# Performance work log

Measured on AMD Instinct MI355X. Metric: run time of the kernel, lower is better.

## Reference

```python
import jax, jax.numpy as jnp
import numpy as np

C = 128; N = 2; H = 64; W = 64; NH = 8
DI = 128; DS = 16; DTR = 8
PE_TEMP = 0.01

def lrelu(x):
    return jnp.where(x >= 0, x, 0.1 * x)

def conv2d(x, w, b, pad):
    y = jax.lax.conv_general_dilated(x, w, (1, 1), [(pad, pad), (pad, pad)],
                                     dimension_numbers=('NCHW', 'OIHW', 'NCHW'))
    return y + b[None, :, None, None]

def _gather2d(img, yy, xx):
    # img (n,c,h,w); yy,xx int32 (n,h,w) -> (n,c,h,w)
    n, c, h, w = img.shape
    idx = (yy * w + xx).reshape(n, 1, h * w)
    g = jnp.take_along_axis(img.reshape(n, c, h * w),
                            jnp.broadcast_to(idx, (n, c, h * w)), axis=2)
    return g.reshape(n, c, h, w)

def bilinear_warp(img, flow):
    # flow (n,2,h,w): [dx, dy]
    n, c, h, w = img.shape
    gy, gx = jnp.meshgrid(jnp.arange(h, dtype=jnp.float32),
                          jnp.arange(w, dtype=jnp.float32), indexing='ij')
    x = gx[None] + flow[:, 0]; y = gy[None] + flow[:, 1]
    x0 = jnp.floor(x); y0 = jnp.floor(y)
    dx = x - x0; dy = y - y0
    x0c = jnp.clip(x0, 0, w - 1).astype(jnp.int32)
    x1c = jnp.clip(x0 + 1, 0, w - 1).astype(jnp.int32)
    y0c = jnp.clip(y0, 0, h - 1).astype(jnp.int32)
    y1c = jnp.clip(y0 + 1, 0, h - 1).astype(jnp.int32)
    wa = ((1 - dx) * (1 - dy))[:, None]; wb = ((1 - dx) * dy)[:, None]
    wc = (dx * (1 - dy))[:, None]; wd = (dx * dy)[:, None]
    return (wa * _gather2d(img, y0c, x0c) + wb * _gather2d(img, y1c, x0c)
            + wc * _gather2d(img, y0c, x1c) + wd * _gather2d(img, y1c, x1c))

def posenc(rel, dim, temp=PE_TEMP):
    # rel (...,2) -> (...,dim) sinusoidal PE with temperature pe_temp
    d4 = dim // 4
    omega = temp ** (jnp.arange(d4, dtype=jnp.float32) / d4)
    xx = rel[..., 0:1] * omega
    yy = rel[..., 1:2] * omega
    return jnp.concatenate([jnp.sin(xx), jnp.cos(xx), jnp.sin(yy), jnp.cos(yy)], axis=-1)

def spynet_flow(f1, f2, s1w, s1b, s2w, s2b, levels=3):
    # SpyNet-style coarse-to-fine residual flow estimation (frozen weights)
    p1 = [f1]; p2 = [f2]
    for _ in range(levels - 1):
        a = p1[-1]; n, c, h, w = a.shape
        p1.append(a.reshape(n, c, h // 2, 2, w // 2, 2).mean(axis=(3, 5)))
        b_ = p2[-1]
        p2.append(b_.reshape(n, c, h // 2, 2, w // 2, 2).mean(axis=(3, 5)))
    flow = None
    for lvl in range(levels - 1, -1, -1):
        a = p1[lvl]; b_ = p2[lvl]
        n, c, h, w = a.shape
        if flow is None:
            flow = jnp.zeros((n, 2, h, w), jnp.float32)
        else:
            flow = 2.0 * jax.image.resize(flow, (n, 2, h, w), 'bilinear')
        warped = bilinear_warp(b_, flow)
        inp = jnp.concatenate([a, warped, flow], axis=1)
        hh = lrelu(conv2d(inp, s1w, s1b, 1))
        flow = flow + conv2d(hh, s2w, s2b, 1)
    return flow

def implicit_warp(feat_prop, feat_cur, flow, wqw, wqb, wkw, wkb, wvw, wvb, wow, wob):
    # Implicit attention-based warp: for each query pixel, attend over the 4
    # integer neighbors of its flow-displaced position in feat_prop, with
    # sinusoidal PE of sub-pixel offsets. flow: (n,h,w,2)
    n, c, h, w = feat_prop.shape
    hw = h * w; hd = c // NH
    gy, gx = jnp.meshgrid(jnp.arange(h, dtype=jnp.float32),
                          jnp.arange(w, dtype=jnp.float32), indexing='ij')
    sx = gx[None] + flow[..., 0]; sy = gy[None] + flow[..., 1]
    fx = jnp.floor(sx); fy = jnp.floor(sy)
    dx = sx - fx; dy = sy - fy
    feats = []; pes = []
    for oy in (0, 1):
        for ox in (0, 1):
            nx = jnp.clip(fx + ox, 0, w - 1).astype(jnp.int32)
            ny = jnp.clip(fy + oy, 0, h - 1).astype(jnp.int32)
            g = _gather2d(feat_prop, ny, nx).reshape(n, c, hw).transpose(0, 2, 1)
            feats.append(g)
            rel = jnp.stack([ox - dx, oy - dy], axis=-1).reshape(n, hw, 2)
            pes.append(posenc(rel, c))
    nf_ = jnp.stack(feats, axis=2)   # (n,hw,4,c)
    pe = jnp.stack(pes, axis=2)
    qin = feat_cur.reshape(n, c, hw).transpose(0, 2, 1) + posenc(
        jnp.stack([dx, dy], axis=-1).reshape(n, hw, 2), c)
    q = (qin @ wqw.T + wqb).reshape(n, hw, NH, hd)
    k = ((nf_ + pe) @ wkw.T + wkb).reshape(n, hw, 4, NH, hd)
    v = (nf_ @ wvw.T + wvb).reshape(n, hw, 4, NH, hd)
    logits = jnp.einsum('nphd,npkhd->npkh', q, k) / np.float32(np.sqrt(hd))
    attn = jax.nn.softmax(logits, axis=2)
    o = jnp.einsum('npkh,npkhd->nphd', attn, v).reshape(n, hw, c) @ wow.T + wob
    return o.transpose(0, 2, 1).reshape(n, c, h, w)

def mamba_fwd(x, in_w, conv_w, conv_b, xproj_w, dt_w, dt_b, A_log, Dp, out_w):
    # Mamba selective scan, expand=1, d_conv=3, d_state=16. x: (B,L,D)
    Bn, L, D = x.shape
    xz = x @ in_w.T
    xs, z = jnp.split(xz, 2, axis=-1)          # (B,L,DI) each
    xt = xs.transpose(0, 2, 1)                  # (B,DI,L)
    xp = jnp.pad(xt, ((0, 0), (0, 0), (2, 0)))  # causal pad (d_conv-1)
    wk_ = conv_w[:, 0, :]                       # (DI,3) depthwise kernel
    xc = (xp[:, :, 0:L] * wk_[:, 0:1] + xp[:, :, 1:L + 1] * wk_[:, 1:2]
          + xp[:, :, 2:L + 2] * wk_[:, 2:3]) + conv_b[:, None]
    xs = jax.nn.silu(xc).transpose(0, 2, 1)     # (B,L,DI)
    dbc = xs @ xproj_w.T
    dtp = dbc[..., :DTR]
    Bm = dbc[..., DTR:DTR + DS]
    Cm = dbc[..., DTR + DS:]
    dt = jax.nn.softplus(dtp @ dt_w.T + dt_b)   # (B,L,DI)
    A = -jnp.exp(A_log)                          # (DI,DS)

    def step(hc, inp):
        dt_t, B_t, C_t, x_t = inp
        dA = jnp.exp(dt_t[..., None] * A)       # (B,DI,DS)
        hc = dA * hc + (dt_t * x_t)[..., None] * B_t[:, None, :]
        y = jnp.einsum('bds,bs->bd', hc, C_t)
        return hc, y

    h0 = jnp.zeros((Bn, DI, DS), jnp.float32)
    _, ys = jax.lax.scan(step, h0, (dt.transpose(1, 0, 2), Bm.transpose(1, 0, 2),
                                    Cm.transpose(1, 0, 2), xs.transpose(1, 0, 2)))
    y = ys.transpose(1, 0, 2) + xs * Dp
    y = y * jax.nn.silu(z)
    return y @ out_w.T

def _forward(l1, l2, l3, l4, l5, l6, l7,
             conv_rec_w, conv_rec_b, conv3_w, conv3_b, conv1x1_w, conv1x1_b,
             conv13_w, conv13_b, wq_w, wq_b, wk_w, wk_b, wv_w, wv_b, wo_w, wo_b,
             m_in_w, m_conv_w, m_conv_b, m_xproj_w, m_dt_w, m_dt_b, m_Alog, m_D,
             m_out_w, spy1_w, spy1_b, spy2_w, spy2_b):
    ls = [l1, l2, l3, l4, l5, l6, l7]
    lqs = jnp.stack([conv2d(l, conv_rec_w, conv_rec_b, 1) for l in ls], axis=1)
    feats = [lrelu(conv2d(l, conv3_w, conv3_b, 1)) for l in ls]
    n, t, c3, h, w = lqs.shape
    f1 = lqs[:, :-1].reshape(-1, c3, h, w)
    f2 = lqs[:, 1:].reshape(-1, c3, h, w)
    flows = spynet_flow(f1, f2, spy1_w, spy1_b, spy2_w, spy2_b).reshape(n, t - 1, 2, h, w)
    # backward-time propagation over frames [6,5,...,0]; flow[idx]: idx->idx+1
    result = [feats[6]]
    feat_prop = feats[6]
    for i in range(1, 7):
        idx = 6 - i
        fl = flows[:, idx].transpose(0, 2, 3, 1)
        feat_prop = implicit_warp(feat_prop, feats[idx], fl,
                                  wq_w, wq_b, wk_w, wk_b, wv_w, wv_b, wo_w, wo_b)
        result.append(feat_prop)
    feats5 = jnp.stack(result, axis=2)                  # (N,C,7,H,W)
    Bn = feats5.shape[0]
    x_flat = feats5.reshape(Bn, C, 7 * h * w).transpose(0, 2, 1)
    out = mamba_fwd(x_flat, m_in_w, m_conv_w, m_conv_b, m_xproj_w,
                    m_dt_w, m_dt_b, m_Alog, m_D, m_out_w)
    out = out.transpose(0, 2, 1).reshape(Bn, C * 7, h, w)
    out = lrelu(conv2d(out, conv1x1_w, conv1x1_b, 0))
    res = []
    for l, r in zip(ls, feats):
        rr = lrelu(conv2d(jnp.concatenate([r, out], axis=1), conv13_w, conv13_b, 1))
        res.append(l + rr)
    return tuple(res)

def setup_inputs():
    key = jax.random.key(0)
    ks = list(jax.random.split(key, 40))
    def rn(k, shape, scale):
        return (jax.random.normal(k, shape) * scale).astype(jnp.float32)
    def cw(k, o, ci, kh, kw):
        return rn(k, (o, ci, kh, kw), 1.0 / np.sqrt(ci * kh * kw))
    inp = {}
    for i in range(7):
        inp['l%d' % (i + 1)] = rn(ks[i], (N, C, H, W), 1.0)
    inp['conv_rec_w'] = cw(ks[7], 3, C, 3, 3); inp['conv_rec_b'] = jnp.zeros((3,), jnp.float32)
    inp['conv3_w'] = cw(ks[8], C, C, 3, 3); inp['conv3_b'] = jnp.zeros((C,), jnp.float32)
    inp['conv1x1_w'] = cw(ks[9], C, C * 7, 1, 1); inp['conv1x1_b'] = jnp.zeros((C,), jnp.float32)
    inp['conv13_w'] = cw(ks[10], C, 2 * C, 3, 3); inp['conv13_b'] = jnp.zeros((C,), jnp.float32)
    sc = 1.0 / np.sqrt(C)
    for j, nm in enumerate(['wq', 'wk', 'wv', 'wo']):
        inp[nm + '_w'] = rn(ks[11 + j], (C, C), sc)
        inp[nm + '_b'] = jnp.zeros((C,), jnp.float32)
    inp['m_in_w'] = rn(ks[15], (2 * DI, C), sc)
    inp['m_conv_w'] = rn(ks[16], (DI, 1, 3), 1.0 / np.sqrt(3))
    inp['m_conv_b'] = jnp.zeros((DI,), jnp.float32)
    inp['m_xproj_w'] = rn(ks[17], (DTR + 2 * DS, DI), sc)
    inp['m_dt_w'] = rn(ks[18], (DI, DTR), 1.0 / np.sqrt(DTR))
    inp['m_dt_b'] = jnp.full((DI,), -4.6, jnp.float32)
    inp['m_Alog'] = jnp.log(jnp.broadcast_to(jnp.arange(1, DS + 1, dtype=jnp.float32), (DI, DS)))
    inp['m_D'] = jnp.ones((DI,), jnp.float32)
    inp['m_out_w'] = rn(ks[19], (C, DI), sc)
    inp['spy1_w'] = cw(ks[20], 32, 8, 3, 3); inp['spy1_b'] = jnp.zeros((32,), jnp.float32)
    inp['spy2_w'] = cw(ks[21], 2, 32, 3, 3); inp['spy2_b'] = jnp.zeros((2,), jnp.float32)
    return inp

def reference(l1, l2, l3, l4, l5, l6, l7,
              conv_rec_w, conv_rec_b, conv3_w, conv3_b, conv1x1_w, conv1x1_b,
              conv13_w, conv13_b, wq_w, wq_b, wk_w, wk_b, wv_w, wv_b, wo_w, wo_b,
              m_in_w, m_conv_w, m_conv_b, m_xproj_w, m_dt_w, m_dt_b, m_Alog, m_D,
              m_out_w, spy1_w, spy1_b, spy2_w, spy2_b):
    return _forward(l1, l2, l3, l4, l5, l6, l7,
                    conv_rec_w, conv_rec_b, conv3_w, conv3_b, conv1x1_w, conv1x1_b,
                    conv13_w, conv13_b, wq_w, wq_b, wk_w, wk_b, wv_w, wv_b, wo_w, wo_b,
                    m_in_w, m_conv_w, m_conv_b, m_xproj_w, m_dt_w, m_dt_b, m_Alog, m_D,
                    m_out_w, spy1_w, spy1_b, spy2_w, spy2_b)
```

## Files before the change

kernel.cpp:

```cpp
#include <hip/hip_runtime.h>
#include <hip/hip_bf16.h>
#include <math.h>

#define NB   2
#define CH   128
#define HT   64
#define WD   64
#define HW   4096
#define TF   7
#define LSEQ 28672
#define NCHUNK 128
#define LCHUNK 224

typedef long long i64;
typedef float f32x4 __attribute__((ext_vector_type(4)));
typedef short sv8 __attribute__((ext_vector_type(8)));
typedef short sv4 __attribute__((ext_vector_type(4)));

struct Ptr7 { const float* p[7]; };

static inline int cdiv(i64 a, int b) { return (int)((a + b - 1) / b); }

__device__ __forceinline__ float lrelu_f(float v) { return v >= 0.f ? v : 0.1f * v; }

__device__ __forceinline__ short bf16r(float f) {
    unsigned u = __float_as_uint(f);
    unsigned r = (u + 0x7FFFu + ((u >> 16) & 1u)) >> 16;
    return (short)r;
}

__global__ void transpose_k(const float* __restrict__ src, float* __restrict__ dst, int R, int Cc) {
    i64 idx = (i64)blockIdx.x * blockDim.x + threadIdx.x;
    if (idx >= (i64)R * Cc) return;
    int r = (int)(idx / Cc), c = (int)(idx - (i64)r * Cc);
    dst[(i64)c * R + r] = src[idx];
}

__global__ void wprep_k(const float* __restrict__ w, short* __restrict__ wb, int CinT, int CC) {
    int idx = blockIdx.x * 256 + threadIdx.x;
    int total = 9 * CC * 8192;
    if (idx >= total) return;
    int e   = idx & 7;
    int cgp = (idx >> 3) & 7;
    int co  = (idx >> 6) & 127;
    int rest = idx >> 13;
    int cc = rest % CC, k9 = rest / CC;
    int cg = cgp ^ (co & 7);
    int ci = cc * 64 + cg * 8 + e;
    wb[idx] = bf16r(w[((i64)co * CinT + ci) * 9 + k9]);
}

__global__ __launch_bounds__(256) void tprep_k(Ptr7 lin, short* __restrict__ tin) {
    __shared__ short st[128 * 130];
    const int tid = threadIdx.x;
    const int pg = blockIdx.x;
    const int z = blockIdx.y; const int t = z >> 1, b = z & 1;
    const float* src = lin.p[t] + (i64)b * 128 * HW + pg * 128;
    int p_ = tid & 127, cihalf = tid >> 7;
    for (int ci0 = 0; ci0 < 128; ci0 += 2) {
        int ci = ci0 + cihalf;
        st[p_ * 130 + ci] = bf16r(src[(i64)ci * HW + p_]);
    }
    __syncthreads();
    for (int it = 0; it < 32; ++it) {
        int o = it * 256 + tid;
        int p = o >> 6, cp = o & 63;
        *(int*)&tin[((i64)z * HW + pg * 128 + p) * 128 + cp * 2] = *(int*)&st[p * 130 + cp * 2];
    }
}

__global__ __launch_bounds__(256) void convmfma_k(
    const short* __restrict__ srcA, const short* __restrict__ srcB, int CC, int chA,
    const short* __restrict__ WB, const float* __restrict__ bias,
    Ptr7 res, int has_res,
    float* __restrict__ outf, short* __restrict__ outb, int relu)
{
    __shared__ short SA[264 * 64];
    __shared__ short SB[128 * 64];
    const int tid = threadIdx.x;
    const int rp = blockIdx.x;
    const int z = blockIdx.y;
    const int t = z >> 1, b = z & 1;
    const int y0 = rp * 2;
    const int pbase = rp * 128;
    const int lane = tid & 63, wv = tid >> 6;
    const int wm = wv & 1, wn = wv >> 1;
    const int l15 = lane & 15, l4 = lane >> 4;

    f32x4 acc[4][4];
    f32x4 zz = {0.f, 0.f, 0.f, 0.f};
// ... 54 lines not shown
        }
    }
    const float* rptr = has_res ? (res.p[t] + (i64)b * 128 * HW) : nullptr;
#pragma unroll
    for (int mt = 0; mt < 4; ++mt) {
        int co0 = wm * 64 + mt * 16 + l4 * 4;
#pragma unroll
        for (int nt = 0; nt < 4; ++nt) {
            int pix = pbase + wn * 64 + nt * 16 + l15;
            float vv[4];
#pragma unroll
            for (int r = 0; r < 4; ++r) {
                float x = acc[mt][nt][r] + bias[co0 + r];
                if (relu) x = lrelu_f(x);
                if (rptr) x += rptr[(i64)(co0 + r) * HW + pix];
                outf[((i64)z * 128 + co0 + r) * HW + pix] = x;
                vv[r] = x;
            }
            if (outb) {
                sv4 pk;
#pragma unroll
                for (int r = 0; r < 4; ++r) pk[r] = bf16r(vv[r]);
                *(sv4*)&outb[((i64)z * HW + pix) * 128 + co0] = pk;
            }
        }
    }
}

__global__ __launch_bounds__(256) void convrec_k(Ptr7 lin, const float* __restrict__ w,
                                                 const float* __restrict__ bias, float* __restrict__ lqs) {
    __shared__ float s_in[16][18][18];
    __shared__ float s_w[3][16][9];
    const int tid = threadIdx.x;
    const int tx = tid & 15, ty = tid >> 4;
    const int tile = blockIdx.x;
    const int z = blockIdx.y; const int t = z >> 1, b = z & 1;
    const int tx0 = (tile & 3) << 4, ty0 = (tile >> 2) << 4;
    const float* in = lin.p[t] + (i64)b * 128 * HW;
    float acc[3] = {bias[0], bias[1], bias[2]};
    for (int ci0 = 0; ci0 < 128; ci0 += 16) {
        for (int idx = tid; idx < 16 * 324; idx += 256) {
            int chn = idx / 324; int r = idx - chn * 324;
            int iy = r / 18; int ix = r - iy * 18;
            int gy = ty0 + iy - 1, gx = tx0 + ix - 1;
            float v = 0.f;
            if (gy >= 0 && gy < 64 && gx >= 0 && gx < 64)
// ... 146 lines not shown
        inp[((i64)bf * 8 + c) * hw + r] = a[((i64)bf * 3 + c) * hw + r];
        inp[((i64)bf * 8 + 3 + c) * hw + r] = wv;
    }
    inp[((i64)bf * 8 + 6) * hw + r] = fx;
    inp[((i64)bf * 8 + 7) * hw + r] = fy;
}

__global__ void resize_flow_k(const float* __restrict__ in, float* __restrict__ out, int hi, int wi) {
    int ho = hi * 2, wo = wi * 2;
    int idx = blockIdx.x * blockDim.x + threadIdx.x;
    if (idx >= 12 * 2 * ho * wo) return;
    int x = idx % wo; int y = (idx / wo) % ho; int c = idx / (wo * ho);
    float py = fminf(fmaxf(0.5f * y - 0.25f, 0.f), (float)(hi - 1));
    float px = fminf(fmaxf(0.5f * x - 0.25f, 0.f), (float)(wi - 1));
    int y0 = (int)py; int x0 = (int)px;
    int y1 = min(y0 + 1, hi - 1); int x1 = min(x0 + 1, wi - 1);
    float dy = py - y0, dx = px - x0;
    const float* ip = in + (i64)c * hi * wi;
    float v = (1.f - dy) * ((1.f - dx) * ip[y0 * wi + x0] + dx * ip[y0 * wi + x1]) +
              dy * ((1.f - dx) * ip[y1 * wi + x0] + dx * ip[y1 * wi + x1]);
    out[idx] = 2.f * v;
}

__global__ void copy_slot0_k(const float* __restrict__ f6, float* __restrict__ f5) {
    i64 idx = (i64)blockIdx.x * blockDim.x + threadIdx.x;
    if (idx >= (i64)NB * CH * HW) return;
    int p = (int)(idx & 4095); i64 bc = idx >> 12;
    f5[bc * (i64)TF * HW + p] = f6[idx];
}

__global__ __launch_bounds__(128) void attn_k(
    const float* __restrict__ prop, i64 pbs, i64 pcs,
    const float* __restrict__ cur,
    const float* __restrict__ flows, int fidx,
    const float* __restrict__ wq_t, const float* __restrict__ wq_b,
    const float* __restrict__ wk_t, const float* __restrict__ wk_b,
    const float* __restrict__ wv_t, const float* __restrict__ wv_b,
    const float* __restrict__ wo_t, const float* __restrict__ wo_b,
    float* __restrict__ outp, i64 obs, i64 ocs)
{
    __shared__ float s_q[8][128];
    __shared__ float s_k[8][4][128];
    __shared__ float s_v[8][4][128];
    __shared__ float s_att[8][4][8];
    __shared__ float s_dx[8], s_dy[8];
    __shared__ int s_nx[8][2], s_ny[8][2];
    const int tid = threadIdx.x;
    const int b = blockIdx.y;
    const int p0 = blockIdx.x * 8;

    if (tid < 8) {
        int p = p0 + tid;
        int gx = p & 63, gy = p >> 6;
        float fx = flows[((i64)(b * 6 + fidx) * 2) * HW + p];
        float fy = flows[((i64)(b * 6 + fidx) * 2 + 1) * HW + p];
        float sx = gx + fx, sy = gy + fy;
        float fxf = floorf(sx), fyf = floorf(sy);
        s_dx[tid] = sx - fxf; s_dy[tid] = sy - fyf;
        s_nx[tid][0] = (int)fminf(fmaxf(fxf, 0.f), 63.f);
        s_nx[tid][1] = (int)fminf(fmaxf(fxf + 1.f, 0.f), 63.f);
        s_ny[tid][0] = (int)fminf(fmaxf(fyf, 0.f), 63.f);
        s_ny[tid][1] = (int)fminf(fmaxf(fyf + 1.f, 0.f), 63.f);
// ... 135 lines not shown
        }
        __syncthreads();
#pragma unroll
        for (int px = 0; px < 8; ++px) s_q[px][tid] = ov[px];
        __syncthreads();
    }
    {
        float oa[8];
#pragma unroll
        for (int i = 0; i < 8; ++i) oa[i] = 0.f;
        for (int j = 0; j < 128; j += 4) {
            float w0 = wo_t[(j    ) * 128 + tid];
            float w1 = wo_t[(j + 1) * 128 + tid];
            float w2 = wo_t[(j + 2) * 128 + tid];
            float w3 = wo_t[(j + 3) * 128 + tid];
#pragma unroll
            for (int px = 0; px < 8; ++px) {
                const float4 x = *(const float4*)&s_q[px][j];
                oa[px] = fmaf(w0, x.x, fmaf(w1, x.y, fmaf(w2, x.z, fmaf(w3, x.w, oa[px]))));
            }
        }
        float bo = wo_b[tid];
#pragma unroll
        for (int px = 0; px < 8; ++px)
            outp[(i64)b * obs + (i64)tid * ocs + (p0 + px)] = oa[px] + bo;
    }
}

__global__ void linear_k(
    const float* __restrict__ X, i64 xb, i64 xl, i64 xk, int kmajor,
    const float* __restrict__ Wt, const float* __restrict__ bias,
    float* __restrict__ Y, int Lr, int K, int O, int act)
{
    extern __shared__ float sx[];
    const int tid = threadIdx.x;
    const int r0 = blockIdx.x * 16;
    const int b = r0 / Lr; const int l0 = r0 - b * Lr;
    const int stride = K + 4;
    for (int idx = tid; idx < 16 * K; idx += blockDim.x) {
        int p, k;
        if (kmajor) { k = idx >> 4; p = idx & 15; }
        else { p = idx / K; k = idx - p * K; }
        sx[p * stride + k] = X[(i64)b * xb + (i64)(l0 + p) * xl + (i64)k * xk];
    }
    __syncthreads();
    if (tid < O) {
        float acc[16];
#pragma unroll
        for (int i = 0; i < 16; ++i) acc[i] = 0.f;
        for (int j = 0; j < K; j += 4) {
            float w0 = Wt[(i64)(j    ) * O + tid];
            float w1 = Wt[(i64)(j + 1) * O + tid];
            float w2 = Wt[(i64)(j + 2) * O + tid];
            float w3 = Wt[(i64)(j + 3) * O + tid];
#pragma unroll
            for (int p = 0; p < 16; ++p) {
                const float4 x = *(const float4*)&sx[p * stride + j];
                acc[p] = fmaf(w0, x.x, fmaf(w1, x.y, fmaf(w2, x.z, fmaf(w3, x.w, acc[p]))));
            }
        }
        float bv = bias ? bias[tid] : 0.f;
#pragma unroll
        for (int p = 0; p < 16; ++p) {
            float v = acc[p] + bv;
            if (act == 1) v = fmaxf(v, 0.f) + log1pf(expf(-fabsf(v)));
            Y[(i64)(r0 + p) * O + tid] = v;
        }
    }
}

__global__ void conv1d_k(const float* __restrict__ xz, const float* __restrict__ cw,
                         const float* __restrict__ cb, float* __restrict__ xs)
{
    i64 idx = (i64)blockIdx.x * blockDim.x + threadIdx.x;
    if (idx >= (i64)NB * LSEQ * 128) return;
    int d = (int)(idx & 127);
    i64 r = idx >> 7;
    i64 l = r % LSEQ;
    float v = cb[d] + cw[d * 3 + 2] * xz[r * 256 + d];
    if (l >= 1) v += cw[d * 3 + 1] * xz[(r - 1) * 256 + d];
    if (l >= 2) v += cw[d * 3    ] * xz[(r - 2) * 256 + d];
    xs[r * 128 + d] = v / (1.f + expf(-v));
}

__global__ __launch_bounds__(256) void scan1_k(
    const float* __restrict__ dtb, const float* __restrict__ xsb,
    const float* __restrict__ dbc, const float* __restrict__ Alog,
    float* __restrict__ HEND, float* __restrict__ SDT)
{
    const int tid = threadIdx.x;
    const int pair = blockIdx.x * 16 + (tid >> 4);
    const int s = tid & 15;
    const int b = pair >> 7, d = pair & 127;
    const int ch = blockIdx.y;
    const i64 lbase = (i64)b * LSEQ + (i64)ch * LCHUNK;
    const float a2 = -expf(Alog[d * 16 + s]) * 1.4426950408889634f;
    const float* dtp = dtb + lbase * 128 + d;
    const float* xsp = xsb + lbase * 128 + d;
    const float* Bp  = dbc + lbase * 40 + 8 + s;
    float h = 0.f, sdt = 0.f;
    for (int t = 0; t < LCHUNK; ++t) {
        float dtv = dtp[(i64)t * 128];
        float xsv = xsp[(i64)t * 128];
        float Bv  = Bp[(i64)t * 40];
        h = fmaf(exp2f(dtv * a2), h, dtv * xsv * Bv);
        sdt += dtv;
    }
    HEND[(((i64)b * NCHUNK + ch) * 128 + d) * 16 + s] = h;
    if (s == 0) SDT[((i64)b * NCHUNK + ch) * 128 + d] = sdt;
}

__global__ void scan2_k(const float* __restrict__ HEND, const float* __restrict__ SDT,
                        const float* __restrict__ Alog, float* __restrict__ HSTART)
{
    int idx = blockIdx.x * 256 + threadIdx.x;
    int b = idx >> 11, d = (idx >> 4) & 127, s = idx & 15;
    float a2 = -expf(Alog[d * 16 + s]) * 1.4426950408889634f;
    float hs = 0.f;
    for (int ch = 0; ch < NCHUNK; ++ch) {
        i64 base = ((i64)b * NCHUNK + ch) * 128 + d;
        HSTART[base * 16 + s] = hs;
        hs = fmaf(exp2f(SDT[base] * a2), hs, HEND[base * 16 + s]);
    }
}

__global__ __launch_bounds__(256) void scan3_k(
    float* __restrict__ dtb,
    const float* __restrict__ xsb, const float* __restrict__ dbc,
    const float* __restrict__ Alog, const float* __restrict__ HSTART,
    const float* __restrict__ xz, const float* __restrict__ Dp)
{
    const int tid = threadIdx.x;
    const int pair = blockIdx.x * 16 + (tid >> 4);
    const int s = tid & 15;
    const int b = pair >> 7, d = pair & 127;
    const int ch = blockIdx.y;
    const i64 lbase = (i64)b * LSEQ + (i64)ch * LCHUNK;
    const float a2 = -expf(Alog[d * 16 + s]) * 1.4426950408889634f;
    float* dtp = dtb + lbase * 128 + d;
    const float* xsp = xsb + lbase * 128 + d;
    const float* Bp  = dbc + lbase * 40 + 8 + s;
    const float* Cp  = dbc + lbase * 40 + 24 + s;
    float h = HSTART[(((i64)b * NCHUNK + ch) * 128 + d) * 16 + s];
    const float dp = Dp[d];
    for (int t = 0; t < LCHUNK; ++t) {
        float dtv = dtp[(i64)t * 128];
        float xsv = xsp[(i64)t * 128];
        float Bv  = Bp[(i64)t * 40];
        float Cv  = Cp[(i64)t * 40];
        h = fmaf(exp2f(dtv * a2), h, dtv * xsv * Bv);
        float yc = h * Cv;
        yc += __shfl_xor(yc, 1, 16);
        yc += __shfl_xor(yc, 2, 16);
        yc += __shfl_xor(yc, 4, 16);
        yc += __shfl_xor(yc, 8, 16);
        if (s == 0) {
            float zv = xz[(lbase + t) * 256 + 128 + d];
            float yf = (yc + xsv * dp) * (zv / (1.f + expf(-zv)));
            dtp[(i64)t * 128] = yf;
        }
    }
}

__global__ __launch_bounds__(128) void conv1x1_k(
    const float* __restrict__ mo, const float* __restrict__ w1t,
    const float* __restrict__ b1, float* __restrict__ out128, short* __restrict__ toutb)
{
    __shared__ float sx[4][896];
    const int tid = threadIdx.x;
    const int b = blockIdx.y;
    const int p0 = blockIdx.x * 4;
#pragma unroll
    for (int px = 0; px < 4; ++px) {
        int p = p0 + px;
#pragma unroll
        for (int t = 0; t < 7; ++t)
            sx[px][tid * 7 + t] = mo[((i64)b * LSEQ + t * HW + p) * 128 + tid];
    }
    __syncthreads();
    float acc[4] = {0.f, 0.f, 0.f, 0.f};
    for (int j = 0; j < 896; j += 4) {
        float w0 = w1t[(j    ) * 128 + tid];
        float w1 = w1t[(j + 1) * 128 + tid];
        float w2 = w1t[(j + 2) * 128 + tid];
        float w3 = w1t[(j + 3) * 128 + tid];
#pragma unroll
        for (int px = 0; px < 4; ++px) {
            const float4 x = *(const float4*)&sx[px][j];
            acc[px] = fmaf(w0, x.x, fmaf(w1, x.y, fmaf(w2, x.z, fmaf(w3, x.w, acc[px]))));
        }
    }
    float bv = b1[tid];
#pragma unroll
    for (int px = 0; px < 4; ++px) {
        float v = lrelu_f(acc[px] + bv);
        out128[((i64)b * 128 + tid) * HW + (p0 + px)] = v;
        toutb[((i64)b * HW + p0 + px) * 128 + tid] = bf16r(v);
    }
}

extern "C" void kernel_launch(void* const* d_in, const int* in_sizes, int n_in,
                              void* d_out, int out_size, void* d_ws, size_t ws_size,
                              hipStream_t stream) {
    (void)in_sizes; (void)n_in; (void)out_size; (void)ws_size;
    const float* Lin[7];
    for (int i = 0; i < 7; ++i) Lin[i] = (const float*)d_in[i];
    const float* conv_rec_w = (const float*)d_in[7];
    const float* conv_rec_b = (const float*)d_in[8];
    const float* conv3_w    = (const float*)d_in[9];
    const float* conv3_b    = (const float*)d_in[10];
    const float* conv1x1_w  = (const float*)d_in[11];
    const float* conv1x1_b  = (const float*)d_in[12];
    const float* conv13_w   = (const float*)d_in[13];
    const float* conv13_b   = (const float*)d_in[14];
    const float* wq_w = (const float*)d_in[15]; const float* wq_b = (const float*)d_in[16];
    const float* wk_w = (const float*)d_in[17]; const float* wk_b = (const float*)d_in[18];
    const float* wv_w = (const float*)d_in[19]; const float* wv_b = (const float*)d_in[20];
    const float* wo_w = (const float*)d_in[21]; const float* wo_b = (const float*)d_in[22];
    const float* m_in_w    = (const float*)d_in[23];
    const float* m_conv_w  = (const float*)d_in[24];
    const float* m_conv_b  = (const float*)d_in[25];
    const float* m_xproj_w = (const float*)d_in[26];
    const float* m_dt_w    = (const float*)d_in[27];
    const float* m_dt_b    = (const float*)d_in[28];
    const float* m_Alog    = (const float*)d_in[29];
    const float* m_D       = (const float*)d_in[30];
    const float* m_out_w   = (const float*)d_in[31];
    const float* spy1_w = (const float*)d_in[32]; const float* spy1_b = (const float*)d_in[33];
    const float* spy2_w = (const float*)d_in[34]; const float* spy2_b = (const float*)d_in[35];
    float* out = (float*)d_out;
    float* W = (float*)d_ws;

    Ptr7 P7; for (int i = 0; i < 7; ++i) P7.p[i] = Lin[i];

    i64 off = 0;
    float* FEATS  = W + off; off += (i64)TF * NB * CH * HW;
    float* FEATS5 = W + off; off += (i64)NB * CH * TF * HW;
    float* XZ     = W + off; off += (i64)NB * LSEQ * 256;
    float* XS     = W + off; off += (i64)NB * LSEQ * 128;
    float* DBC    = W + off; off += (i64)NB * LSEQ * 40;
    float* DT     = W + off; off += (i64)NB * LSEQ * 128;
    float* OUT128 = W + off; off += (i64)NB * 128 * HW;
    float* WQ_T = W + off; off += 16384;
    float* WK_T = W + off; off += 16384;
    float* WV_T = W + off; off += 16384;
    float* WO_T = W + off; off += 16384;
    float* MIN_T  = W + off; off += 256 * 128;
    float* MXP_T  = W + off; off += 40 * 128;
    float* MDT_T  = W + off; off += 128 * 8;
    float* MOUT_T = W + off; off += 16384;
    float* W1_T   = W + off; off += 128 * 896;
    float* LQS  = W + off; off += (i64)NB * TF * 3 * HW;
    float* P1_0 = W + off; off += 12 * 3 * HW;
    float* P2_0 = W + off; off += 12 * 3 * HW;
    float* P1_1 = W + off; off += 12 * 3 * 1024;
    float* P2_1 = W + off; off += 12 * 3 * 1024;
    float* P1_2 = W + off; off += 12 * 3 * 256;
    float* P2_2 = W + off; off += 12 * 3 * 256;
    float* FLOW2 = W + off; off += 12 * 2 * 256;
    float* FLOW1 = W + off; off += 12 * 2 * 1024;
    float* FLOW0 = W + off; off += 12 * 2 * HW;
    float* INP = W + off; off += 12 * 8 * HW;
    float* HHB = W + off; off += 12 * 32 * HW;
    float* HEND   = W + off; off += (i64)NB * NCHUNK * 128 * 16;
    float* HSTART = W + off; off += (i64)NB * NCHUNK * 128 * 16;
    float* SDT    = W + off; off += (i64)NB * NCHUNK * 128;
    float* MO = XZ;
    short* SBASE = (short*)(W + off);
    i64 soff = 0;
    short* TIN    = SBASE + soff; soff += (i64)14 * HW * 128;
    short* TFEATS = SBASE + soff; soff += (i64)14 * HW * 128;
    short* TOUT   = SBASE + soff; soff += (i64)NB * HW * 128;
    short* WB3    = SBASE + soff; soff += (i64)9 * 2 * 8192;
    short* WB13   = SBASE + soff; soff += (i64)9 * 4 * 8192;

    auto T = [&](const float* src, float* dst, int R, int Cc) {
        transpose_k<<<cdiv((i64)R * Cc, 256), 256, 0, stream>>>(src, dst, R, Cc);
    };
    T(wq_w, WQ_T, 128, 128); T(wk_w, WK_T, 128, 128);
    T(wv_w, WV_T, 128, 128); T(wo_w, WO_T, 128, 128);
    T(m_in_w, MIN_T, 256, 128); T(m_xproj_w, MXP_T, 40, 128);
    T(m_dt_w, MDT_T, 128, 8);   T(m_out_w, MOUT_T, 128, 128);
    T(conv1x1_w, W1_T, 128, 896);
    wprep_k<<<cdiv(9 * 2 * 8192, 256), 256, 0, stream>>>(conv3_w, WB3, 128, 2);
    wprep_k<<<cdiv(9 * 4 * 8192, 256), 256, 0, stream>>>(conv13_w, WB13, 256, 4);
    tprep_k<<<dim3(32, 14), 256, 0, stream>>>(P7, TIN);

    convrec_k<<<dim3(16, 14), 256, 0, stream>>>(P7, conv_rec_w, conv_rec_b, LQS);

    {
        Ptr7 none; for (int i = 0; i < 7; ++i) none.p[i] = nullptr;
        convmfma_k<<<dim3(32, 14), 256, 0, stream>>>(
            TIN, nullptr, 2, 2, WB3, conv3_b, none, 0, FEATS, TFEATS, 1);
    }

    copy_pyr_k<<<cdiv(12 * 3 * HW, 256), 256, 0, stream>>>(LQS, P1_0, 0);
    copy_pyr_k<<<cdiv(12 * 3 * HW, 256), 256, 0, stream>>>(LQS, P2_0, 1);
    avgpool_k<<<cdiv(36 * 32 * 32, 256), 256, 0, stream>>>(P1_0, P1_1, 36, 64, 64);
    avgpool_k<<<cdiv(36 * 32 * 32, 256), 256, 0, stream>>>(P2_0, P2_1, 36, 64, 64);
    avgpool_k<<<cdiv(36 * 16 * 16, 256), 256, 0, stream>>>(P1_1, P1_2, 36, 32, 32);
    avgpool_k<<<cdiv(36 * 16 * 16, 256), 256, 0, stream>>>(P2_1, P2_2, 36, 32, 32);
    hipMemsetAsync(FLOW2, 0, 12 * 2 * 256 * sizeof(float), stream);

    struct Lvl { float *p1, *p2, *fl; int hw_; };
    Lvl lv[3] = { {P1_2, P2_2, FLOW2, 16}, {P1_1, P2_1, FLOW1, 32}, {P1_0, P2_0, FLOW0, 64} };
    for (int li = 0; li < 3; ++li) {
        int hl = lv[li].hw_;
        int hw = hl * hl;
        int tiles = (hl / 16) * (hl / 16);
        build_inp_k<<<cdiv(12 * hw, 256), 256, 0, stream>>>(lv[li].p1, lv[li].p2, lv[li].fl, INP, hl, hl);
        conv3x3_k<<<dim3(tiles, 2, 12), 256, 0, stream>>>(
            INP, 8, (i64)8 * hw, nullptr, 0, 0, spy1_w, spy1_b, 32, hl, hl,
            nullptr, 0, HHB, (i64)32 * hw, 1);
        conv3x3_k<<<dim3(tiles, 1, 12), 256, 0, stream>>>(
            HHB, 32, (i64)32 * hw, nullptr, 0, 0, spy2_w, spy2_b, 2, hl, hl,
            lv[li].fl, (i64)2 * hw, lv[li].fl, (i64)2 * hw, 0);
        if (li < 2) {
            int ho = hl * 2;
            resize_flow_k<<<cdiv(12 * 2 * ho * ho, 256), 256, 0, stream>>>(lv[li].fl, lv[li + 1].fl, hl, hl);
        }
    }

    copy_slot0_k<<<cdiv((i64)NB * CH * HW, 256), 256, 0, stream>>>(FEATS + 6LL * NB * CH * HW, FEATS5);
    for (int i = 1; i <= 6; ++i) {
        int fidx = 6 - i;
        const float* cur = FEATS + (i64)fidx * NB * CH * HW;
        const float* prop; i64 pbs, pcs;
        if (i == 1) { prop = FEATS + 6LL * NB * CH * HW; pbs = (i64)CH * HW; pcs = HW; }
        else { prop = FEATS5 + (i64)(i - 1) * HW; pbs = (i64)CH * TF * HW; pcs = (i64)TF * HW; }
        attn_k<<<dim3(512, 2), 128, 0, stream>>>(
            prop, pbs, pcs, cur, FLOW0, fidx,
            WQ_T, wq_b, WK_T, wk_b, WV_T, wv_b, WO_T, wo_b,
            FEATS5 + (i64)i * HW, (i64)CH * TF * HW, (i64)TF * HW);
    }

    const int nrow_blocks = (NB * LSEQ) / 16;
    linear_k<<<nrow_blocks, 256, 16 * (128 + 4) * 4, stream>>>(
        FEATS5, (i64)CH * LSEQ, 1, LSEQ, 1, MIN_T, nullptr, XZ, LSEQ, 128, 256, 0);
    conv1d_k<<<cdiv((i64)NB * LSEQ * 128, 256), 256, 0, stream>>>(XZ, m_conv_w, m_conv_b, XS);
    linear_k<<<nrow_blocks, 64, 16 * (128 + 4) * 4, stream>>>(
        XS, (i64)LSEQ * 128, 128, 1, 0, MXP_T, nullptr, DBC, LSEQ, 128, 40, 0);
    linear_k<<<nrow_blocks, 128, 16 * (8 + 4) * 4, stream>>>(
        DBC, (i64)LSEQ * 40, 40, 1, 0, MDT_T, m_dt_b, DT, LSEQ, 8, 128, 1);
    scan1_k<<<dim3(16, NCHUNK), 256, 0, stream>>>(DT, XS, DBC, m_Alog, HEND, SDT);
    scan2_k<<<16, 256, 0, stream>>>(HEND, SDT, m_Alog, HSTART);
    scan3_k<<<dim3(16, NCHUNK), 256, 0, stream>>>(DT, XS, DBC, m_Alog, HSTART, XZ, m_D);
    linear_k<<<nrow_blocks, 128, 16 * (128 + 4) * 4, stream>>>(
        DT, (i64)LSEQ * 128, 128, 1, 0, MOUT_T, nullptr, MO, LSEQ, 128, 128, 0);
    conv1x1_k<<<dim3(1024, 2), 128, 0, stream>>>(MO, W1_T, conv1x1_b, OUT128, TOUT);

    convmfma_k<<<dim3(32, 14), 256, 0, stream>>>(
        TFEATS, TOUT, 4, 2, WB13, conv13_b, P7, 1, out, nullptr, 1);
}
```

Baseline: 1.616 ms.

## Move Mamba linears and 1x1 conv to bf16 MFMA GEMMs, restructure scan

Replaces the fp32 linear_k projections (in, x-proj, out) and the conv1x1 kernel with a shared bf16 MFMA tiled GEMM kernel. Producers such as attention, slot copy, conv1d and scan3 now also write bf16 token-major copies to feed these GEMMs. The selective scan changes from one thread per (d,s) with shuffle reductions to one thread per channel holding all 16 states in registers, with more, shorter chunks. This cuts FP32 ALU work and memory traffic at the cost of bf16 rounding in the projections.

```diff
diff --git a/kernel.cpp b/kernel.cpp
--- a/kernel.cpp
+++ b/kernel.cpp
@@ -9,8 +9,8 @@
 #define HW   4096
 #define TF   7
 #define LSEQ 28672
-#define NCHUNK 128
-#define LCHUNK 224
+#define NCHUNK 448
+#define LCHUNK 64
 
 typedef long long i64;
 typedef float f32x4 __attribute__((ext_vector_type(4)));
@@ -50,6 +50,25 @@
     wb[idx] = bf16r(w[((i64)co * CinT + ci) * 9 + k9]);
 }
 
+__global__ void wgprep_k(const float* __restrict__ w, short* __restrict__ wb,
+                         int K, int O, int nblk, int kmapmode, int total) {
+    int idx = blockIdx.x * 256 + threadIdx.x;
+    if (idx >= total) return;
+    int e = idx & 7;
+    int cgp = (idx >> 3) & 7;
+    int co = (idx >> 6) & 127;
+    int chunk = idx >> 13;
+    int blk = chunk % nblk, kc = chunk / nblk;
+    int cop = blk * 128 + co;
+    int k = kc * 64 + ((cgp ^ (co & 7)) * 8) + e;
+    float v = 0.f;
+    if (cop < O && k < K) {
+        int sk = (kmapmode == 1) ? ((k & 127) * 7 + (k >> 7)) : k;
+        v = w[(i64)cop * K + sk];
+    }
+    wb[idx] = bf16r(v);
+}
+
 __global__ __launch_bounds__(256) void tprep_k(Ptr7 lin, short* __restrict__ tin) {
     __shared__ short st[128 * 130];
     const int tid = threadIdx.x;
@@ -66,6 +85,26 @@
         int o = it * 256 + tid;
         int p = o >> 6, cp = o & 63;
         *(int*)&tin[((i64)z * HW + pg * 128 + p) * 128 + cp * 2] = *(int*)&st[p * 130 + cp * 2];
+    }
+}
+
+__global__ __launch_bounds__(256) void slot0_k(const float* __restrict__ f6, short* __restrict__ tf5) {
+    __shared__ short st[128 * 130];
+    const int tid = threadIdx.x;
+    const int pg = blockIdx.x;
+    const int b = blockIdx.y;
+    const float* src = f6 + (i64)b * 128 * HW + pg * 128;
+    int p_ = tid & 127, chalf = tid >> 7;
+    for (int c0 = 0; c0 < 128; c0 += 2) {
+        int c = c0 + chalf;
+        st[p_ * 130 + c] = bf16r(src[(i64)c * HW + p_]);
+    }
+    __syncthreads();
+    short* dst = tf5 + ((i64)(b * 7) * HW + (i64)pg * 128) * 128;
+    for (int it = 0; it < 32; ++it) {
+        int o = it * 256 + tid;
+        int p = o >> 6, cp = o & 63;
+        *(int*)&dst[(i64)p * 128 + cp * 2] = *(int*)&st[p * 130 + cp * 2];
     }
 }
 
@@ -166,6 +205,96 @@
 #pragma unroll
                 for (int r = 0; r < 4; ++r) pk[r] = bf16r(vv[r]);
                 *(sv4*)&outb[((i64)z * HW + pix) * 128 + co0] = pk;
+            }
+        }
+    }
+}
+
+__global__ __launch_bounds__(256) void gemm_k(
+    const short* __restrict__ A, i64 lda, int Kc, int nblk,
+    const short* __restrict__ WB, const float* __restrict__ bias, int Ovalid,
+    float* __restrict__ outf, i64 ldo,
+    short* __restrict__ outb, int mode)
+{
+    __shared__ short SA[128 * 64];
+    __shared__ short SB[128 * 64];
+    const int tid = threadIdx.x;
+    const i64 row0 = (i64)blockIdx.x * 128;
+    const int blk = blockIdx.y;
+    const int lane = tid & 63, wv = tid >> 6;
+    const int wm = wv & 1, wn = wv >> 1;
+    const int l15 = lane & 15, l4 = lane >> 4;
+
+    f32x4 acc[4][4];
+    f32x4 zz = {0.f, 0.f, 0.f, 0.f};
+#pragma unroll
+    for (int i = 0; i < 4; ++i)
+#pragma unroll
+        for (int j = 0; j < 4; ++j) acc[i][j] = zz;
+
+    for (int kc = 0; kc < Kc; ++kc) {
+        __syncthreads();
+        {
+            const short* ap = A + row0 * lda + kc * 64;
+#pragma unroll
+            for (int it = 0; it < 4; ++it) {
+                int idx = it * 256 + tid;
+                int r = idx >> 3, cg = idx & 7;
+                int4 val = *(const int4*)(ap + (i64)r * lda + cg * 8);
+                *(int4*)&SA[r * 64 + ((cg ^ (r & 7)) * 8)] = val;
+            }
+            const short* wsrc = WB + (i64)(kc * nblk + blk) * 8192;
+#pragma unroll
+            for (int it = 0; it < 4; ++it) {
+                int o = it * 256 + tid;
+                *(int4*)&SB[o * 8] = *(const int4*)(wsrc + o * 8);
+            }
+        }
+        __syncthreads();
+#pragma unroll
+        for (int ks = 0; ks < 2; ++ks) {
+            sv8 af[4], bfr[4];
+            int cgk = ks * 4 + l4;
+#pragma unroll
+            for (int mt = 0; mt < 4; ++mt) {
+                int co = wm * 64 + mt * 16 + l15;
+                af[mt] = *(const sv8*)&SB[co * 64 + ((cgk ^ (co & 7)) * 8)];
+            }
+#pragma unroll
+            for (int nt = 0; nt < 4; ++nt) {
+                int rr = wn * 64 + nt * 16 + l15;
+                bfr[nt] = *(const sv8*)&SA[rr * 64 + ((cgk ^ (rr & 7)) * 8)];
+            }
+#pragma unroll
+            for (int mt = 0; mt < 4; ++mt)
+#pragma unroll
+                for (int nt = 0; nt < 4; ++nt)
+                    acc[mt][nt] = __builtin_amdgcn_mfma_f32_16x16x32_bf16(af[mt], bfr[nt], acc[mt][nt], 0, 0, 0);
+        }
+    }
+#pragma unroll
+    for (int mt = 0; mt < 4; ++mt) {
+        int co0 = wm * 64 + mt * 16 + l4 * 4;
+#pragma unroll
+        for (int nt = 0; nt < 4; ++nt) {
+            i64 row = row0 + wn * 64 + nt * 16 + l15;
+#pragma unroll
+            for (int r = 0; r < 4; ++r) {
+                int c = co0 + r;
+                float v = acc[mt][nt][r];
+                if (mode == 0) {
+                    if (c < Ovalid) {
+                        if (bias) v += bias[blk * 128 + c];
+                        outf[row * ldo + blk * 128 + c] = v;
+                    }
+                } else if (mode == 1) {
+                    int b = (int)(row / LSEQ); int rem = (int)(row - (i64)b * LSEQ);
+                    int t7 = rem >> 12, p = rem & 4095;
+                    outb[((i64)(b * HW + p)) * 896 + t7 * 128 + c] = bf16r(v);
+                } else {
+                    v = lrelu_f(v + bias[c]);
+                    outb[row * 128 + c] = bf16r(v);
+                }
             }
         }
     }
@@ -358,13 +487,6 @@
     out[idx] = 2.f * v;
 }
 
-__global__ void copy_slot0_k(const float* __restrict__ f6, float* __restrict__ f5) {
-    i64 idx = (i64)blockIdx.x * blockDim.x + threadIdx.x;
-    if (idx >= (i64)NB * CH * HW) return;
-    int p = (int)(idx & 4095); i64 bc = idx >> 12;
-    f5[bc * (i64)TF * HW + p] = f6[idx];
-}
-
 __global__ __launch_bounds__(128) void attn_k(
     const float* __restrict__ prop, i64 pbs, i64 pcs,
     const float* __restrict__ cur,
@@ -373,7 +495,8 @@
     const float* __restrict__ wk_t, const float* __restrict__ wk_b,
     const float* __restrict__ wv_t, const float* __restrict__ wv_b,
     const float* __restrict__ wo_t, const float* __restrict__ wo_b,
-    float* __restrict__ outp, i64 obs, i64 ocs)
+    float* __restrict__ outp, i64 obs, i64 ocs,
+    short* __restrict__ tf5, int slot)
 {
     __shared__ float s_q[8][128];
     __shared__ float s_k[8][4][128];
@@ -555,8 +678,11 @@
         }
         float bo = wo_b[tid];
 #pragma unroll
-        for (int px = 0; px < 8; ++px)
-            outp[(i64)b * obs + (i64)tid * ocs + (p0 + px)] = oa[px] + bo;
+        for (int px = 0; px < 8; ++px) {
+            float v = oa[px] + bo;
+            outp[(i64)b * obs + (i64)tid * ocs + (p0 + px)] = v;
+            tf5[(((i64)(b * 7 + slot)) * HW + (p0 + px)) * 128 + tid] = bf16r(v);
+        }
     }
 }
 
@@ -603,7 +729,8 @@
 }
 
 __global__ void conv1d_k(const float* __restrict__ xz, const float* __restrict__ cw,
-                         const float* __restrict__ cb, float* __restrict__ xs)
+                         const float* __restrict__ cb, float* __restrict__ xs,
+                         short* __restrict__ xsb)
 {
     i64 idx = (i64)blockIdx.x * blockDim.x + threadIdx.x;
     if (idx >= (i64)NB * LSEQ * 128) return;
@@ -613,122 +740,124 @@
     float v = cb[d] + cw[d * 3 + 2] * xz[r * 256 + d];
     if (l >= 1) v += cw[d * 3 + 1] * xz[(r - 1) * 256 + d];
     if (l >= 2) v += cw[d * 3    ] * xz[(r - 2) * 256 + d];
-    xs[r * 128 + d] = v / (1.f + expf(-v));
-}
-
-__global__ __launch_bounds__(256) void scan1_k(
+    float sv = v / (1.f + expf(-v));
+    xs[r * 128 + d] = sv;
+    xsb[r * 128 + d] = bf16r(sv);
+}
+
+#define LOG2E 1.4426950408889634f
+
+__global__ __launch_bounds__(128) void scan1_k(
     const float* __restrict__ dtb, const float* __restrict__ xsb,
     const float* __restrict__ dbc, const float* __restrict__ Alog,
     float* __restrict__ HEND, float* __restrict__ SDT)
 {
-    const int tid = threadIdx.x;
-    const int pair = blockIdx.x * 16 + (tid >> 4);
-    const int s = tid & 15;
-    const int b = pair >> 7, d = pair & 127;
-    const int ch = blockIdx.y;
+    const int d = threadIdx.x;
+    const int ch = blockIdx.x, b = blockIdx.y;
     const i64 lbase = (i64)b * LSEQ + (i64)ch * LCHUNK;
-    const float a2 = -expf(Alog[d * 16 + s]) * 1.4426950408889634f;
-    const float* dtp = dtb + lbase * 128 + d;
-    const float* xsp = xsb + lbase * 128 + d;
-    const float* Bp  = dbc + lbase * 40 + 8 + s;
-    float h = 0.f, sdt = 0.f;
+    float a2[16];
+    {
+        const float4* ap = (const float4*)(Alog + d * 16);
+#pragma unroll
+        for (int i = 0; i < 4; ++i) {
+            float4 av = ap[i];
+            a2[i * 4 + 0] = -expf(av.x) * LOG2E;
+            a2[i * 4 + 1] = -expf(av.y) * LOG2E;
+            a2[i * 4 + 2] = -expf(av.z) * LOG2E;
+            a2[i * 4 + 3] = -expf(av.w) * LOG2E;
+        }
+    }
+    float h[16];
+#pragma unroll
+    for (int i = 0; i < 16; ++i) h[i] = 0.f;
+    float sdt = 0.f;
     for (int t = 0; t < LCHUNK; ++t) {
-        float dtv = dtp[(i64)t * 128];
-        float xsv = xsp[(i64)t * 128];
-        float Bv  = Bp[(i64)t * 40];
-        h = fmaf(exp2f(dtv * a2), h, dtv * xsv * Bv);
+        i64 l = lbase + t;
+        float dtv = dtb[l * 128 + d];
+        float xsv = xsb[l * 128 + d];
+        const float4* Bp = (const float4*)(dbc + l * 40 + 8);
+        float4 B0 = Bp[0], B1 = Bp[1], B2 = Bp[2], B3 = Bp[3];
+        float dtxs = dtv * xsv;
+        float bs[16] = {B0.x, B0.y, B0.z, B0.w, B1.x, B1.y, B1.z, B1.w,
+                        B2.x, B2.y, B2.z, B2.w, B3.x, B3.y, B3.z, B3.w};
+#pragma unroll
+        for (int s = 0; s < 16; ++s)
+            h[s] = fmaf(exp2f(dtv * a2[s]), h[s], dtxs * bs[s]);
         sdt += dtv;
     }
-    HEND[(((i64)b * NCHUNK + ch) * 128 + d) * 16 + s] = h;
-    if (s == 0) SDT[((i64)b * NCHUNK + ch) * 128 + d] = sdt;
-}
-
-__global__ void scan2_k(const float* __restrict__ HEND, const float* __restrict__ SDT,
-                        const float* __restrict__ Alog, float* __restrict__ HSTART)
+    i64 cb = (i64)b * NCHUNK + ch;
+#pragma unroll
+    for (int s = 0; s < 16; ++s) HEND[(cb * 16 + s) * 128 + d] = h[s];
+    SDT[cb * 128 + d] = sdt;
+}
+
+__global__ void scan2_k(float* __restrict__ HH, const float* __restrict__ SDT,
+                        const float* __restrict__ Alog)
 {
     int idx = blockIdx.x * 256 + threadIdx.x;
-    int b = idx >> 11, d = (idx >> 4) & 127, s = idx & 15;
-    float a2 = -expf(Alog[d * 16 + s]) * 1.4426950408889634f;
+    int b = idx >> 11, s = (idx >> 7) & 15, d = idx & 127;
+    float a2 = -expf(Alog[d * 16 + s]) * LOG2E;
     float hs = 0.f;
     for (int ch = 0; ch < NCHUNK; ++ch) {
-        i64 base = ((i64)b * NCHUNK + ch) * 128 + d;
-        HSTART[base * 16 + s] = hs;
-        hs = fmaf(exp2f(SDT[base] * a2), hs, HEND[base * 16 + s]);
-    }
-}
-
-__global__ __launch_bounds__(256) void scan3_k(
-    float* __restrict__ dtb,
-    const float* __restrict__ xsb, const float* __restrict__ dbc,
-    const float* __restrict__ Alog, const float* __restrict__ HSTART,
-    const float* __restrict__ xz, const float* __restrict__ Dp)
+        i64 cb = (i64)b * NCHUNK + ch;
+        i64 base = (cb * 16 + s) * 128 + d;
+        float he = HH[base];
+        HH[base] = hs;
+        hs = fmaf(exp2f(SDT[cb * 128 + d] * a2), hs, he);
+    }
+}
+
+__global__ __launch_bounds__(128) void scan3_k(
+    const float* __restrict__ dtb, const float* __restrict__ xsb,
+    const float* __restrict__ dbc, const float* __restrict__ Alog,
+    const float* __restrict__ HSTART,
+    const float* __restrict__ xz, const float* __restrict__ Dp,
+    short* __restrict__ yb)
 {
-    const int tid = threadIdx.x;
-    const int pair = blockIdx.x * 16 + (tid >> 4);
-    const int s = tid & 15;
-    const int b = pair >> 7, d = pair & 127;
-    const int ch = blockIdx.y;
+    const int d = threadIdx.x;
+    const int ch = blockIdx.x, b = blockIdx.y;
     const i64 lbase = (i64)b * LSEQ + (i64)ch * LCHUNK;
-    const float a2 = -expf(Alog[d * 16 + s]) * 1.4426950408889634f;
-    float* dtp = dtb + lbase * 128 + d;
-    const float* xsp = xsb + lbase * 128 + d;
-    const float* Bp  = dbc + lbase * 40 + 8 + s;
-    const float* Cp  = dbc + lbase * 40 + 24 + s;
-    float h = HSTART[(((i64)b * NCHUNK + ch) * 128 + d) * 16 + s];
+    float a2[16];
+    {
+        const float4* ap = (const float4*)(Alog + d * 16);
+#pragma unroll
+        for (int i = 0; i < 4; ++i) {
+            float4 av = ap[i];
+            a2[i * 4 + 0] = -expf(av.x) * LOG2E;
+            a2[i * 4 + 1] = -expf(av.y) * LOG2E;
+            a2[i * 4 + 2] = -expf(av.z) * LOG2E;
+            a2[i * 4 + 3] = -expf(av.w) * LOG2E;
+        }
+    }
+    const i64 cb = (i64)b * NCHUNK + ch;
+    float h[16];
+#pragma unroll
+    for (int s = 0; s < 16; ++s) h[s] = HSTART[(cb * 16 + s) * 128 + d];
     const float dp = Dp[d];
     for (int t = 0; t < LCHUNK; ++t) {
-        float dtv = dtp[(i64)t * 128];
-        float xsv = xsp[(i64)t * 128];
-        float Bv  = Bp[(i64)t * 40];
-        float Cv  = Cp[(i64)t * 40];
-        h = fmaf(exp2f(dtv * a2), h, dtv * xsv * Bv);
-        float yc = h * Cv;
-        yc += __shfl_xor(yc, 1, 16);
-        yc += __shfl_xor(yc, 2, 16);
-        yc += __shfl_xor(yc, 4, 16);
-        yc += __shfl_xor(yc, 8, 16);
-        if (s == 0) {
-            float zv = xz[(lbase + t) * 256 + 128 + d];
-            float yf = (yc + xsv * dp) * (zv / (1.f + expf(-zv)));
-            dtp[(i64)t * 128] = yf;
-        }
-    }
-}
-
-__global__ __launch_bounds__(128) void conv1x1_k(
-    const float* __restrict__ mo, const float* __restrict__ w1t,
-    const float* __restrict__ b1, float* __restrict__ out128, short* __restrict__ toutb)
-{
-    __shared__ float sx[4][896];
-    const int tid = threadIdx.x;
-    const int b = blockIdx.y;
-    const int p0 = blockIdx.x * 4;
-#pragma unroll
-    for (int px = 0; px < 4; ++px) {
-        int p = p0 + px;
-#pragma unroll
-        for (int t = 0; t < 7; ++t)
-            sx[px][tid * 7 + t] = mo[((i64)b * LSEQ + t * HW + p) * 128 + tid];
-    }
-    __syncthreads();
-    float acc[4] = {0.f, 0.f, 0.f, 0.f};
-    for (int j = 0; j < 896; j += 4) {
-        float w0 = w1t[(j    ) * 128 + tid];
-        float w1 = w1t[(j + 1) * 128 + tid];
-        float w2 = w1t[(j + 2) * 128 + tid];
-        float w3 = w1t[(j + 3) * 128 + tid];
-#pragma unroll
-        for (int px = 0; px < 4; ++px) {
-            const float4 x = *(const float4*)&sx[px][j];
-            acc[px] = fmaf(w0, x.x, fmaf(w1, x.y, fmaf(w2, x.z, fmaf(w3, x.w, acc[px]))));
-        }
-    }
-    float bv = b1[tid];
-#pragma unroll
-    for (int px = 0; px < 4; ++px) {
-        float v = lrelu_f(acc[px] + bv);
-        out128[((i64)b * 128 + tid) * HW + (p0 + px)] = v;
-        toutb[((i64)b * HW + p0 + px) * 128 + tid] = bf16r(v);
+        i64 l = lbase + t;
+        float dtv = dtb[l * 128 + d];
+        float xsv = xsb[l * 128 + d];
+        const float4* Bp = (const float4*)(dbc + l * 40 + 8);
+        float4 B0 = Bp[0], B1 = Bp[1], B2 = Bp[2], B3 = Bp[3];
+        const float4* Cp = (const float4*)(dbc + l * 40 + 24);
+        float4 C0 = Cp[0], C1 = Cp[1], C2 = Cp[2], C3 = Cp[3];
+        float dtxs = dtv * xsv;
+        float bs[16] = {B0.x, B0.y, B0.z, B0.w, B1.x, B1.y, B1.z, B1.w,
+                        B2.x, B2.y, B2.z, B2.w, B3.x, B3.y, B3.z, B3.w};
+        float cs[16] = {C0.x, C0.y, C0.z, C0.w, C1.x, C1.y, C1.z, C1.w,
+                        C2.x, C2.y, C2.z, C2.w, C3.x, C3.y, C3.z, C3.w};
+#pragma unroll
+        for (int s = 0; s < 16; ++s)
+            h[s] = fmaf(exp2f(dtv * a2[s]), h[s], dtxs * bs[s]);
+        float y0 = fmaf(h[3], cs[3], fmaf(h[2], cs[2], fmaf(h[1], cs[1], h[0] * cs[0])));
+        float y1 = fmaf(h[7], cs[7], fmaf(h[6], cs[6], fmaf(h[5], cs[5], h[4] * cs[4])));
+        float y2 = fmaf(h[11], cs[11], fmaf(h[10], cs[10], fmaf(h[9], cs[9], h[8] * cs[8])));
+        float y3 = fmaf(h[15], cs[15], fmaf(h[14], cs[14], fmaf(h[13], cs[13], h[12] * cs[12])));
+        float yc = (y0 + y1) + (y2 + y3);
+        float zv = xz[l * 256 + 128 + d];
+        float yf = (yc + xsv * dp) * (zv / (1.f + expf(-zv)));
+        yb[l * 128 + d] = bf16r(yf);
     }
 }
 
@@ -773,16 +902,11 @@
     float* XS     = W + off; off += (i64)NB * LSEQ * 128;
     float* DBC    = W + off; off += (i64)NB * LSEQ * 40;
     float* DT     = W + off; off += (i64)NB * LSEQ * 128;
-    float* OUT128 = W + off; off += (i64)NB * 128 * HW;
     float* WQ_T = W + off; off += 16384;
     float* WK_T = W + off; off += 16384;
     float* WV_T = W + off; off += 16384;
     float* WO_T = W + off; off += 16384;
-    float* MIN_T  = W + off; off += 256 * 128;
-    float* MXP_T  = W + off; off += 40 * 128;
     float* MDT_T  = W + off; off += 128 * 8;
-    float* MOUT_T = W + off; off += 16384;
-    float* W1_T   = W + off; off += 128 * 896;
     float* LQS  = W + off; off += (i64)NB * TF * 3 * HW;
     float* P1_0 = W + off; off += 12 * 3 * HW;
     float* P2_0 = W + off; off += 12 * 3 * HW;
@@ -795,10 +919,8 @@
     float* FLOW0 = W + off; off += 12 * 2 * HW;
     float* INP = W + off; off += 12 * 8 * HW;
     float* HHB = W + off; off += 12 * 32 * HW;
-    float* HEND   = W + off; off += (i64)NB * NCHUNK * 128 * 16;
-    float* HSTART = W + off; off += (i64)NB * NCHUNK * 128 * 16;
+    float* HEND   = W + off; off += (i64)NB * NCHUNK * 16 * 128;
     float* SDT    = W + off; off += (i64)NB * NCHUNK * 128;
-    float* MO = XZ;
     short* SBASE = (short*)(W + off);
     i64 soff = 0;
     short* TIN    = SBASE + soff; soff += (i64)14 * HW * 128;
@@ -806,17 +928,28 @@
     short* TOUT   = SBASE + soff; soff += (i64)NB * HW * 128;
     short* WB3    = SBASE + soff; soff += (i64)9 * 2 * 8192;
     short* WB13   = SBASE + soff; soff += (i64)9 * 4 * 8192;
+    short* WGIN   = SBASE + soff; soff += 2 * 2 * 8192;
+    short* WGXP   = SBASE + soff; soff += 2 * 1 * 8192;
+    short* WGOUT  = SBASE + soff; soff += 2 * 1 * 8192;
+    short* WG11   = SBASE + soff; soff += 14 * 1 * 8192;
+    short* XSB = TIN;
+    short* TF5 = (short*)DT;
+    short* YB  = (short*)FEATS;
+    short* MO2 = (short*)XZ;
+    float* HSTART = HEND;
 
     auto T = [&](const float* src, float* dst, int R, int Cc) {
         transpose_k<<<cdiv((i64)R * Cc, 256), 256, 0, stream>>>(src, dst, R, Cc);
     };
     T(wq_w, WQ_T, 128, 128); T(wk_w, WK_T, 128, 128);
     T(wv_w, WV_T, 128, 128); T(wo_w, WO_T, 128, 128);
-    T(m_in_w, MIN_T, 256, 128); T(m_xproj_w, MXP_T, 40, 128);
-    T(m_dt_w, MDT_T, 128, 8);   T(m_out_w, MOUT_T, 128, 128);
-    T(conv1x1_w, W1_T, 128, 896);
+    T(m_dt_w, MDT_T, 128, 8);
     wprep_k<<<cdiv(9 * 2 * 8192, 256), 256, 0, stream>>>(conv3_w, WB3, 128, 2);
     wprep_k<<<cdiv(9 * 4 * 8192, 256), 256, 0, stream>>>(conv13_w, WB13, 256, 4);
+    wgprep_k<<<cdiv(2 * 2 * 8192, 256), 256, 0, stream>>>(m_in_w,    WGIN,  128, 256, 2, 0, 2 * 2 * 8192);
+    wgprep_k<<<cdiv(2 * 1 * 8192, 256), 256, 0, stream>>>(m_xproj_w, WGXP,  128, 40,  1, 0, 2 * 1 * 8192);
+    wgprep_k<<<cdiv(2 * 1 * 8192, 256), 256, 0, stream>>>(m_out_w,   WGOUT, 128, 128, 1, 0, 2 * 1 * 8192);
+    wgprep_k<<<cdiv(14 * 8192, 256), 256, 0, stream>>>(conv1x1_w, WG11, 896, 128, 1, 1, 14 * 8192);
     tprep_k<<<dim3(32, 14), 256, 0, stream>>>(P7, TIN);
 
     convrec_k<<<dim3(16, 14), 256, 0, stream>>>(P7, conv_rec_w, conv_rec_b, LQS);
@@ -854,7 +987,7 @@
         }
     }
 
-    copy_slot0_k<<<cdiv((i64)NB * CH * HW, 256), 256, 0, stream>>>(FEATS + 6LL * NB * CH * HW, FEATS5);
+    slot0_k<<<dim3(32, NB), 256, 0, stream>>>(FEATS + 6LL * NB * CH * HW, TF5);
     for (int i = 1; i <= 6; ++i) {
         int fidx = 6 - i;
         const float* cur = FEATS + (i64)fidx * NB * CH * HW;
@@ -864,23 +997,20 @@
         attn_k<<<dim3(512, 2), 128, 0, stream>>>(
             prop, pbs, pcs, cur, FLOW0, fidx,
             WQ_T, wq_b, WK_T, wk_b, WV_T, wv_b, WO_T, wo_b,
-            FEATS5 + (i64)i * HW, (i64)CH * TF * HW, (i64)TF * HW);
-    }
-
-    const int nrow_blocks = (NB * LSEQ) / 16;
-    linear_k<<<nrow_blocks, 256, 16 * (128 + 4) * 4, stream>>>(
-        FEATS5, (i64)CH * LSEQ, 1, LSEQ, 1, MIN_T, nullptr, XZ, LSEQ, 128, 256, 0);
-    conv1d_k<<<cdiv((i64)NB * LSEQ * 128, 256), 256, 0, stream>>>(XZ, m_conv_w, m_conv_b, XS);
-    linear_k<<<nrow_blocks, 64, 16 * (128 + 4) * 4, stream>>>(
-        XS, (i64)LSEQ * 128, 128, 1, 0, MXP_T, nullptr, DBC, LSEQ, 128, 40, 0);
-    linear_k<<<nrow_blocks, 128, 16 * (8 + 4) * 4, stream>>>(
+            FEATS5 + (i64)i * HW, (i64)CH * TF * HW, (i64)TF * HW,
+            TF5, i);
+    }
+
+    gemm_k<<<dim3(448, 2), 256, 0, stream>>>(TF5, 128, 2, 2, WGIN, nullptr, 128, XZ, 256, nullptr, 0);
+    conv1d_k<<<cdiv((i64)NB * LSEQ * 128, 256), 256, 0, stream>>>(XZ, m_conv_w, m_conv_b, XS, XSB);
+    gemm_k<<<dim3(448, 1), 256, 0, stream>>>(XSB, 128, 2, 1, WGXP, nullptr, 40, DBC, 40, nullptr, 0);
+    linear_k<<<(NB * LSEQ) / 16, 128, 16 * (8 + 4) * 4, stream>>>(
         DBC, (i64)LSEQ * 40, 40, 1, 0, MDT_T, m_dt_b, DT, LSEQ, 8, 128, 1);
-    scan1_k<<<dim3(16, NCHUNK), 256, 0, stream>>>(DT, XS, DBC, m_Alog, HEND, SDT);
-    scan2_k<<<16, 256, 0, stream>>>(HEND, SDT, m_Alog, HSTART);
-    scan3_k<<<dim3(16, NCHUNK), 256, 0, stream>>>(DT, XS, DBC, m_Alog, HSTART, XZ, m_D);
-    linear_k<<<nrow_blocks, 128, 16 * (128 + 4) * 4, stream>>>(
-        DT, (i64)LSEQ * 128, 128, 1, 0, MOUT_T, nullptr, MO, LSEQ, 128, 128, 0);
-    conv1x1_k<<<dim3(1024, 2), 128, 0, stream>>>(MO, W1_T, conv1x1_b, OUT128, TOUT);
+    scan1_k<<<dim3(NCHUNK, NB), 128, 0, stream>>>(DT, XS, DBC, m_Alog, HEND, SDT);
+    scan2_k<<<16, 256, 0, stream>>>(HEND, SDT, m_Alog);
+    scan3_k<<<dim3(NCHUNK, NB), 128, 0, stream>>>(DT, XS, DBC, m_Alog, HSTART, XZ, m_D, YB);
+    gemm_k<<<dim3(448, 1), 256, 0, stream>>>(YB, 128, 2, 1, WGOUT, nullptr, 128, nullptr, 0, MO2, 1);
+    gemm_k<<<dim3(64, 1), 256, 0, stream>>>(MO2, 896, 14, 1, WG11, conv1x1_b, 128, nullptr, 0, TOUT, 2);
 
     convmfma_k<<<dim3(32, 14), 256, 0, stream>>>(
         TFEATS, TOUT, 4, 2, WB13, conv13_b, P7, 1, out, nullptr, 1);
```

Result: faster. 1.322 ms (-18.2%).
